# Kernel optimization log

Measured on AMD Instinct MI355X. Metric: run time of the kernel, lower is better.

Reference implementation:

```python
import jax, jax.numpy as jnp
import numpy as np

V, E, H, B, TE, TD = 32000, 256, 256, 32, 128, 64


def _gru_cell(x, h, Wi, Wh, bi, bh):
    # PyTorch GRU gate order: r, z, n
    gi = x @ Wi.T + bi            # [B, 3H]
    gh = h @ Wh.T + bh            # [B, 3H]
    i_r, i_z, i_n = jnp.split(gi, 3, axis=-1)
    h_r, h_z, h_n = jnp.split(gh, 3, axis=-1)
    r = jax.nn.sigmoid(i_r + h_r)
    z = jax.nn.sigmoid(i_z + h_z)
    n = jnp.tanh(i_n + r * h_n)
    return (1.0 - z) * n + z * h


def _run_gru(x_seq, h0, Wi, Wh, bi, bh, reverse=False):
    # x_seq: [B, T, D] -> outputs [B, T, H]
    xs = jnp.swapaxes(x_seq, 0, 1)  # [T, B, D]
    def step(h, x_t):
        h = _gru_cell(x_t, h, Wi, Wh, bi, bh)
        return h, h
    _, ys = jax.lax.scan(step, h0, xs, reverse=reverse)
    return jnp.swapaxes(ys, 0, 1)


def setup_inputs() -> dict:
    key = jax.random.key(0)
    ks = jax.random.split(key, 22)
    k = 1.0 / np.sqrt(H)
    u = lambda kk, shape, a: jax.random.uniform(kk, shape, jnp.float32, -a, a)
    return {
        'enc_in': jax.random.randint(ks[0], (B, TE), 0, V),
        'dec_in': jax.random.randint(ks[1], (B, TD), 0, V),
        'embed_W': u(ks[2], (V, E), 0.1),
        'Wi_f': u(ks[3], (3 * H, E), k), 'Wh_f': u(ks[4], (3 * H, H), k),
        'bi_f': u(ks[5], (3 * H,), k), 'bh_f': u(ks[6], (3 * H,), k),
        'Wi_b': u(ks[7], (3 * H, E), k), 'Wh_b': u(ks[8], (3 * H, H), k),
        'bi_b': u(ks[9], (3 * H,), k), 'bh_b': u(ks[10], (3 * H,), k),
        'Wi_d': u(ks[11], (3 * H, E + 2 * H), k), 'Wh_d': u(ks[12], (3 * H, H), k),
        'bi_d': u(ks[13], (3 * H,), k), 'bh_d': u(ks[14], (3 * H,), k),
        'W1_w': u(ks[15], (H, 2 * H), 1.0 / np.sqrt(2 * H)), 'W1_b': u(ks[16], (H,), 1.0 / np.sqrt(2 * H)),
        'W2_w': u(ks[17], (2 * H, H), k), 'W2_b': u(ks[18], (2 * H,), k),
        'lin_w': u(ks[19], (V, H), 0.1), 'lin_b': jnp.zeros((V,), jnp.float32),
    }


def reference(enc_in, dec_in, embed_W, Wi_f, Wh_f, bi_f, bh_f, Wi_b, Wh_b, bi_b, bh_b,
              Wi_d, Wh_d, bi_d, bh_d, W1_w, W1_b, W2_w, W2_b, lin_w, lin_b):
    # ---- encoder (bidirectional GRU, 1 layer) ----
    enc_emb = embed_W[enc_in]                                   # [B, TE, E]
    h0 = jnp.zeros((B, H), enc_emb.dtype)
    out_f = _run_gru(enc_emb, h0, Wi_f, Wh_f, bi_f, bh_f)       # [B, TE, H]
    out_b = _run_gru(enc_emb, h0, Wi_b, Wh_b, bi_b, bh_b, reverse=True)
    encoded = jnp.concatenate([out_f, out_b], axis=-1)          # [B, TE, 2H]

    # last valid state per example: encoded[i, sizes[i]-1]
    sizes = (enc_in > 0).sum(axis=1)                            # [B]
    last_states = encoded[jnp.arange(B), sizes - 1]             # [B, 2H]

    # ---- decoder with Luong attention (teacher forcing) ----
    dec_emb = embed_W[dec_in]                                   # [B, TD, E]
    h_init = last_states @ W1_w.T + W1_b                        # [B, H]
    ctx_init = jnp.zeros((B, 2 * H), enc_emb.dtype)

    def dec_step(carry, x_t):
        h, ctx = carry
        inp = jnp.concatenate([ctx, x_t], axis=-1)              # [B, E+2H]
        h = _gru_cell(inp, h, Wi_d, Wh_d, bi_d, bh_d)           # [B, H]
        comp = h @ W2_w.T + W2_b                                # [B, 2H]
        scores = jax.nn.softmax(jnp.einsum('bte,be->bt', encoded, comp), axis=-1)
        ctx = jnp.einsum('bt,bte->be', scores, encoded)          # [B, 2H]
        return (h, ctx), h

    _, outs = jax.lax.scan(dec_step, (h_init, ctx_init), jnp.swapaxes(dec_emb, 0, 1))
    outs = jnp.swapaxes(outs, 0, 1)                             # [B, TD, H]
    logits = outs @ lin_w.T + lin_b                             # [B, TD, V]
    return logits
```

## Files before the change

### kernel.cpp

```cpp
#include <hip/hip_runtime.h>
#include <hip/hip_bf16.h>

#define Vv 32000
#define Ee 256
#define Hh 256
#define Bb 32
#define TEe 128
#define TDd 64

typedef __attribute__((ext_vector_type(4))) float f32x4;
typedef __attribute__((ext_vector_type(8))) short short8;
typedef __attribute__((ext_vector_type(2))) unsigned int uint2v;
typedef __attribute__((ext_vector_type(4))) unsigned int uint4v;

static __device__ __forceinline__ unsigned short f2bf(float f){
  unsigned u = __float_as_uint(f);
  u += 0x7fffu + ((u >> 16) & 1u);
  return (unsigned short)(u >> 16);
}
static __device__ __forceinline__ unsigned pack2(float a, float b){
  return ((unsigned)f2bf(b) << 16) | (unsigned)f2bf(a);
}
static __device__ __forceinline__ float dot8(uint4v u, const float* hh){
  float s = 0.f;
  #pragma unroll
  for (int i = 0; i < 4; ++i){
    unsigned w = u[i];
    s = fmaf(__uint_as_float(w << 16),        hh[2*i],   s);
    s = fmaf(__uint_as_float(w & 0xffff0000u), hh[2*i+1], s);
  }
  return s;
}
static __device__ __forceinline__ float sigmoidf_(float x){
  return 1.f / (1.f + __expf(-x));
}
static __device__ __forceinline__ void gload16(const void* g, void* l){
  __builtin_amdgcn_global_load_lds((const __attribute__((address_space(1))) void*)g,
                                   (__attribute__((address_space(3))) void*)l, 16, 0, 0);
}

__global__ void k_prep(const float* __restrict__ Wh_f, const float* __restrict__ Wh_b,
                       const float* __restrict__ Wh_d,
                       const float* __restrict__ Wi_f, const float* __restrict__ Wi_b,
                       const float* __restrict__ Wi_d, const float* __restrict__ W2_w,
                       unsigned short* __restrict__ whf, unsigned short* __restrict__ whb,
                       unsigned short* __restrict__ whd,
                       unsigned short* __restrict__ wif, unsigned short* __restrict__ wib,
                       unsigned short* __restrict__ wid, unsigned short* __restrict__ w2t){
  int idx = blockIdx.x * 256 + threadIdx.x;
  if (idx < 589824){
    int which = idx / 196608, local = idx % 196608;
    int i = local & 7, r = (local >> 3) % 768, kb = local / 6144;
    const float* src = (which == 0) ? Wh_f : (which == 1) ? Wh_b : Wh_d;
    unsigned short* dst = (which == 0) ? whf : (which == 1) ? whb : whd;
    dst[local] = f2bf(src[(size_t)r*256 + kb*8 + i]);
  } else if (idx < 786432)   wif[idx - 589824] = f2bf(Wi_f[idx - 589824]);
  else if (idx < 983040)     wib[idx - 786432] = f2bf(Wi_b[idx - 786432]);
  else if (idx < 1572864)    wid[idx - 983040] = f2bf(Wi_d[idx - 983040]);
  else if (idx < 1703936){
    int l = idx - 1572864;
    int n = l >> 9, k = l & 511;
    w2t[l] = f2bf(W2_w[k*256 + n]);
  }
}

template<bool A_BF16, bool A_GATHER, bool B_BF16, int OUTMODE>
__global__ __launch_bounds__(256) void k_gemm(
  const void* __restrict__ Av, const int* __restrict__ tokp, const float* __restrict__ embp,
  const void* __restrict__ Bv,
  const float* __restrict__ bias, void* __restrict__ Cv,
  int M, int N, int K, int lda, int ldb, int ldc)
{
  __shared__ unsigned short lA[128*40];
  __shared__ unsigned short lB[128*40];
  const int SA = A_BF16 ? 32 : 40;
  const int SB = B_BF16 ? 32 : 40;
  const int tid  = threadIdx.x;
  const int lane = tid & 63;
  const int wv   = tid >> 6;
  const int w = tid >> 6, wr = w >> 1, wc = w & 1;
  const int m0 = blockIdx.y * 128, n0 = blockIdx.x * 128;
  f32x4 acc[4][4];
  #pragma unroll
  for (int i = 0; i < 4; ++i)
    #pragma unroll
    for (int j = 0; j < 4; ++j) acc[i][j] = (f32x4){0.f,0.f,0.f,0.f};

  for (int k0 = 0; k0 < K; k0 += 32){
    if (A_GATHER){
      #pragma unroll
      for (int it = 0; it < 4; ++it){
        int idx = tid + it*256; int r = idx >> 3, q = idx & 7;
        const float* src = embp + (size_t)tokp[m0 + r]*256 + k0 + q*4;
        f32x4 v = *(const f32x4*)src;
        uint2v pk; pk[0] = pack2(v[0], v[1]); pk[1] = pack2(v[2], v[3]);
        *(uint2v*)&lA[r*40 + q*4] = pk;
      }
    } else if (A_BF16){
      const unsigned short* A = (const unsigned short*)Av;
      #pragma unroll
      for (int i = 0; i < 2; ++i){
        const int rowb = (wv*2 + i)*16;
        gload16(A + (size_t)(m0 + rowb + (lane >> 2))*lda + k0 + (lane & 3)*8,
                &lA[rowb*32]);
      }
    } else {
      const float* A = (const float*)Av;
      #pragma unroll
      for (int it = 0; it < 4; ++it){
        int idx = tid + it*256; int r = idx >> 3, q = idx & 7;
        f32x4 v = *(const f32x4*)(A + (size_t)(m0+r)*lda + k0 + q*4);
        uint2v pk; pk[0] = pack2(v[0], v[1]); pk[1] = pack2(v[2], v[3]);
        *(uint2v*)&lA[r*40 + q*4] = pk;
      }
    }
    if (B_BF16){
      const unsigned short* Bp = (const unsigned short*)Bv;
      #pragma unroll
      for (int i = 0; i < 2; ++i){
        const int rowb = (wv*2 + i)*16;
        gload16(Bp + (size_t)(n0 + rowb + (lane >> 2))*ldb + k0 + (lane & 3)*8,
                &lB[rowb*32]);
      }
    } else {
      const float* Bp = (const float*)Bv;
      #pragma unroll
      for (int it = 0; it < 4; ++it){
        int idx = tid + it*256; int r = idx >> 3, q = idx & 7;
        f32x4 v = *(const f32x4*)(Bp + (size_t)(n0+r)*ldb + k0 + q*4);
        uint2v pk; pk[0] = pack2(v[0], v[1]); pk[1] = pack2(v[2], v[3]);
        *(uint2v*)&lB[r*40 + q*4] = pk;
      }
    }
    __syncthreads();
    short8 av[4], bv[4];
    #pragma unroll
    for (int i = 0; i < 4; ++i)
      av[i] = *(const short8*)&lA[(wr*64 + i*16 + (lane&15))*SA + (lane>>4)*8];
    #pragma unroll
    for (int j = 0; j < 4; ++j)
      bv[j] = *(const short8*)&lB[(wc*64 + j*16 + (lane&15))*SB + (lane>>4)*8];
    #pragma unroll
    for (int i = 0; i < 4; ++i)
      #pragma unroll
      for (int j = 0; j < 4; ++j)
        acc[i][j] = __builtin_amdgcn_mfma_f32_16x16x32_bf16(av[i], bv[j], acc[i][j], 0, 0, 0);
    __syncthreads();
  }
  #pragma unroll
  for (int i = 0; i < 4; ++i){
    #pragma unroll
    for (int j = 0; j < 4; ++j){
      int col = n0 + wc*64 + j*16 + (lane & 15);
      float bb = bias ? bias[col] : 0.f;
      #pragma unroll
      for (int r = 0; r < 4; ++r){
        int row = m0 + wr*64 + i*16 + (lane>>4)*4 + r;
        float v = acc[i][j][r] + bb;
        if (OUTMODE == 2){
          ((unsigned short*)Cv)[(size_t)(row >> 7)*98304 + (size_t)((row & 127) >> 3)*6144
                                + (size_t)col*8 + (row & 7)] = f2bf(v);
        } else if (OUTMODE == 1){
          ((unsigned short*)Cv)[(size_t)row*ldc + col] = f2bf(v);
        } else {
          ((float*)Cv)[(size_t)row*ldc + col] = v;
        }
      }
    }
  }
}

__global__ __launch_bounds__(1024) void k_encoder(
  const unsigned short* __restrict__ Whf, const unsigned short* __restrict__ Whb,
  const float* __restrict__ bhf, const float* __restrict__ bhb,
  const float* __restrict__ gif, const float* __restrict__ gib,
  float* __restrict__ encoded, unsigned short* __restrict__ encoded_bf,
  const float* __restrict__ lin_w, unsigned short* __restrict__ lin_bf, int do_lin)
{
  if (blockIdx.x >= 64){
    if (do_lin){
      const int nlin = Vv*Hh;
      for (int i = (blockIdx.x - 64)*1024 + threadIdx.x; i < nlin; i += 128*1024)
        lin_bf[i] = f2bf(lin_w[i]);
    }
    return;
  }
  extern __shared__ char smem[];
  unsigned short* lw = (unsigned short*)smem;
  float* hA   = (float*)(smem + 131072);
  float* hB   = (float*)(smem + 132096);
  float* parA = (float*)(smem + 133120);
  float* parB = (float*)(smem + 137216);
  const int dir = blockIdx.x & 1, b = blockIdx.x >> 1;
  const unsigned short* Wh = dir ? Whb : Whf;
  const float* bh = dir ? bhb : bhf;
  const float* gi = dir ? gib : gif;
  const int T = threadIdx.x;
  const int rl = T & 255, q4 = T >> 8;
  const int rrh = T & 511, hf = T >> 9;
  const unsigned short* wsrc = Wh + (size_t)(hf*16)*6144 + (size_t)(256 + rrh)*8;
  uint4v wb[8];
  #pragma unroll
  for (int d = 0; d < 8; ++d) wb[d] = *(const uint4v*)(wsrc + (size_t)d*6144);
  for (int cc = T; cc < 256*32; cc += 1024){
    int r = cc >> 5, q = cc & 31;
    *(uint4v*)&lw[(r*32 + (q ^ (r & 31)))*8] = *(const uint4v*)(Wh + (size_t)q*6144 + r*8);
  }
  float bh0 = 0.f, bh1 = 0.f, bh2 = 0.f;
  if (T < 256){ bh0 = bh[T]; bh1 = bh[T+256]; bh2 = bh[T+512]; hA[T] = 0.f; }
  __syncthreads();
  const float* hc = hA; float* hn = hB;
  for (int s = 0; s < TEe; ++s){
    const int t = dir ? (TEe-1-s) : s;
    float g0 = 0.f, g1 = 0.f, g2 = 0.f;
    if (T < 256){
      const float* grow = gi + (size_t)(b*TEe + t)*768;
      g0 = grow[T]; g1 = grow[T+256]; g2 = grow[T+512];
    }
    float aL = 0.f;
    #pragma unroll
    for (int i = 0; i < 8; ++i){
      const int ck = q4*8 + i;
      float hr[8];
      *(f32x4*)&hr[0] = *(const f32x4*)&hc[ck*8];
      *(f32x4*)&hr[4] = *(const f32x4*)&hc[ck*8+4];
      aL += dot8(*(const uint4v*)&lw[(rl*32 + (ck ^ (rl & 31)))*8], hr);
    }
    parA[q4*256 + rl] = aL;
    float aR = 0.f;
    const float* hh = hc + hf*128;
    #pragma unroll
    for (int q = 0; q < 16; ++q){
      float hr[8];
      *(f32x4*)&hr[0] = *(const f32x4*)&hh[q*8];
      *(f32x4*)&hr[4] = *(const f32x4*)&hh[q*8+4];
      aR += dot8(wb[q & 7], hr);
      wb[q & 7] = *(const uint4v*)(wsrc + (size_t)((q < 8) ? (q + 8) : (q - 8))*6144);
    }
    parB[hf*512 + rrh] = aR;
    __syncthreads();
    if (T < 256){
      const int j = T;
      const float A0 = parA[j] + parA[256+j] + parA[512+j] + parA[768+j] + bh0;
      const float A1 = parB[j] + parB[512+j] + bh1;
      const float A2 = parB[256+j] + parB[768+j] + bh2;
      const float r = sigmoidf_(g0 + A0);
      const float z = sigmoidf_(g1 + A1);
      const float n = tanhf(g2 + r*A2);
      const float hnew = (1.f - z)*n + z*hc[j];
      hn[j] = hnew;
      const size_t off = (size_t)(b*TEe + t)*512 + dir*256 + j;
      encoded[off] = hnew;
      encoded_bf[off] = f2bf(hnew);
    }
    __syncthreads();
    const float* tmp = hc; hc = hn; hn = (float*)tmp;
  }
}

__global__ __launch_bounds__(256) void k_post(
  const float* __restrict__ encoded, const float* __restrict__ W2b, float* __restrict__ encb2,
  const int* __restrict__ enc_in, const float* __restrict__ W1w, const float* __restrict__ W1b,
  float* __restrict__ h0)
{
  if (blockIdx.x < 1024){
    const int r = blockIdx.x*4 + (threadIdx.x >> 6), l = threadIdx.x & 63;
    const float* e = encoded + (size_t)r*512;
    float s = 0.f;
    for (int k = l; k < 512; k += 64) s += e[k]*W2b[k];
    for (int off = 32; off; off >>= 1) s += __shfl_down(s, off);
    if (l == 0) encb2[r] = s;
  } else {
    const int b = blockIdx.x - 1024, o = threadIdx.x;
    int c = 0;
    for (int t = 0; t < TEe; ++t) c += (enc_in[b*TEe + t] > 0);
    int idx = c - 1;
    idx = idx < 0 ? 0 : (idx > TEe-1 ? TEe-1 : idx);
    const float* ls = encoded + (size_t)(b*TEe + idx)*512;
    const float* wv = W1w + (size_t)o*512;
    float s = W1b[o];
    for (int k = 0; k < 512; k += 4){
      f32x4 a = *(const f32x4*)(ls + k);
      f32x4 w4 = *(const f32x4*)(wv + k);
      s = fmaf(a[0],w4[0], fmaf(a[1],w4[1], fmaf(a[2],w4[2], fmaf(a[3],w4[3], s))));
    }
    h0[b*256 + o] = s;
  }
}

#define DLR 128
__global__ __launch_bounds__(512, 1) void k_decoder(
  const unsigned short* __restrict__ Whd, const float* __restrict__ bhd,
  const float* __restrict__ gidx,
  const unsigned short* __restrict__ encw2,
  const float* __restrict__ encb2,
  const unsigned short* __restrict__ projt,
  const float* __restrict__ h0,
  unsigned short* __restrict__ outs_bf)
{
  extern __shared__ char smem[];
  unsigned short* le = (unsigned short*)smem;
  unsigned short* lw = (unsigned short*)(smem + 65536);
  float* h    = (float*)(smem + 131072);
  float* parL = (float*)(smem + 132096);
  float* parS1= (float*)(smem + 134144);
  float* parS2= (float*)(smem + 136192);
  float* gcs  = (float*)(smem + 138240);
  float* cpar = (float*)(smem + 140288);
  float* p    = (float*)(smem + 142336);
  float* ebl  = (float*)(smem + 142848);
  const int b = blockIdx.x, T = threadIdx.x;
  const unsigned short* ptc = projt + (size_t)b*98304;
  const unsigned short* wsrcM = Whd + (size_t)(DLR + T)*8;
  const int trow = 640 + (T >> 2), tq = (T & 3)*8;
  const unsigned short* wsrcT = Whd + (size_t)trow*8;
  const unsigned short* csrcM = ptc + (size_t)T*8;
  const int crow = 512 + (T >> 1), cq = (T & 1)*8;
  const unsigned short* csrcT = ptc + (size_t)crow*8;
  uint4v wb[8], wb2[2], cb[4], cb2[2];
  #pragma unroll
  for (int d = 0; d < 8; ++d) wb[d] = *(const uint4v*)(wsrcM + (size_t)d*6144);
  wb2[0] = *(const uint4v*)(wsrcT + (size_t)tq*6144);
  wb2[1] = *(const uint4v*)(wsrcT + (size_t)(tq+1)*6144);
  #pragma unroll
  for (int d = 0; d < 4; ++d) cb[d] = *(const uint4v*)(csrcM + (size_t)d*6144);
  cb2[0] = *(const uint4v*)(csrcT + (size_t)cq*6144);
  cb2[1] = *(const uint4v*)(csrcT + (size_t)(cq+1)*6144);
  for (int cc = T; cc < 128*32; cc += 512){
    int r = cc >> 5, q = cc & 31;
    *(uint4v*)&le[(r*32 + (q ^ (r & 31)))*8] =
        *(const uint4v*)(encw2 + ((size_t)(b*TEe + r) << 8) + (q << 3));
  }
  for (int cc = T; cc < DLR*32; cc += 512){
    int r = cc >> 5, q = cc & 31;
    *(uint4v*)&lw[(r*32 + (q ^ (r & 31)))*8] =
        *(const uint4v*)(Whd + (size_t)q*6144 + r*8);
  }
  for (int i = T; i < 256; i += 512) h[i] = h0[b*256 + i];
  gcs[T] = 0.f; cpar[T] = 0.f;
  if (T < TEe) ebl[T] = encb2[b*TEe + T];
  float bh0 = 0.f, bh1 = 0.f, bh2 = 0.f;
  if (T < 256){ bh0 = bhd[T]; bh1 = bhd[T+256]; bh2 = bhd[T+512]; }
  __syncthreads();
  float g0 = 0.f, g1 = 0.f, g2 = 0.f;
  if (T < 256){
    const float* grow = gidx + (size_t)(b*TDd)*768;
    g0 = grow[T]; g1 = grow[T+256]; g2 = grow[T+512];
  }
  #define DOTS_BODY                                                            \
  {                                                                            \
    { const int rL2 = T >> 2, qb2 = (T & 3)*8;                                 \
      const unsigned short* lwr = lw + rL2*256;                                \
      float a = 0.f;                                                           \
      _Pragma("unroll")                                                        \
      for (int i = 0; i < 8; ++i){                                             \
        const int q = qb2 + i;                                                 \
        float hr[8];                                                           \
        *(f32x4*)&hr[0] = *(const f32x4*)&h[q*8];                              \
        *(f32x4*)&hr[4] = *(const f32x4*)&h[q*8+4];                            \
        a += dot8(*(const uint4v*)(lwr + ((q ^ (rL2 & 31)) << 3)), hr);        \
      }                                                                        \
      parL[(T & 3)*128 + rL2] = a;                                             \
    }                                                                          \
    { float a = 0.f;                                                           \
      _Pragma("unroll")                                                        \
      for (int q = 0; q < 32; ++q){                                            \
        float hr[8];                                                           \
        *(f32x4*)&hr[0] = *(const f32x4*)&h[q*8];                              \
        *(f32x4*)&hr[4] = *(const f32x4*)&h[q*8+4];                            \
        a += dot8(wb[q & 7], hr);                                              \
        wb[q & 7] = *(const uint4v*)(wsrcM + (size_t)((q < 24) ? (q + 8) : (q - 24))*6144); \
      }                                                                        \
      parS1[T] = a;                                                            \
    }                                                                          \
    { float a = 0.f;                                                           \
      _Pragma("unroll")                                                        \
      for (int i = 0; i < 8; ++i){                                             \
        const int q = tq + i;                                                  \
        float hr[8];                                                           \
        *(f32x4*)&hr[0] = *(const f32x4*)&h[q*8];                              \
        *(f32x4*)&hr[4] = *(const f32x4*)&h[q*8+4];                            \
        a += dot8(wb2[i & 1], hr);                                             \
        wb2[i & 1] = *(const uint4v*)(wsrcT + (size_t)(tq + ((i < 6) ? (i + 2) : (i - 6)))*6144); \
      }                                                                        \
      parS2[(T & 3)*128 + (T >> 2)] = a;                                       \
    }                                                                          \
  }
  DOTS_BODY
  __syncthreads();
  for (int t = 0; t < TDd; ++t){
    if (T < 256){
      const int j = T;
      float A0, A2;
      if (j < 128){
        A0 = parL[j] + parL[128+j] + parL[256+j] + parL[384+j];
        A2 = parS1[384+j];
      } else {
        A0 = parS1[j-128];
        A2 = parS2[j-128] + parS2[j] + parS2[j+128] + parS2[j+256];
      }
      const float A1 = parS1[128+j];
      const float gcr = gcs[j];
      const float gcz = gcs[256+j];
      const float gcn = cpar[j] + cpar[256+j];
      const float r = sigmoidf_(g0 + gcr + A0 + bh0);
      const float z = sigmoidf_(g1 + gcz + A1 + bh1);
      const float n = tanhf(g2 + gcn + r*(A2 + bh2));
      const float hnew = (1.f - z)*n + z*h[j];
      h[j] = hnew;
      outs_bf[(size_t)(b*TDd + t)*256 + j] = f2bf(hnew);
    }
    if (t + 1 == TDd) break;
    __syncthreads();
    if (T < 256){
      const float* grow = gidx + (size_t)(b*TDd + t + 1)*768;
      g0 = grow[T]; g1 = grow[T+256]; g2 = grow[T+512];
    }
    DOTS_BODY
    {
      const int pos = T >> 2, kq = (T & 3)*8;
      const unsigned short* er = le + pos*256;
      float s = 0.f;
      #pragma unroll
      for (int i = 0; i < 8; ++i){
        const int q = kq + i;
        float hr[8];
        *(f32x4*)&hr[0] = *(const f32x4*)&h[q*8];
        *(f32x4*)&hr[4] = *(const f32x4*)&h[q*8+4];
        s += dot8(*(const uint4v*)(er + ((q ^ (pos & 31)) << 3)), hr);
      }
      s += __shfl_xor(s, 1);
      s += __shfl_xor(s, 2);
      if ((T & 3) == 0) p[pos] = s + ebl[pos];
    }
    __syncthreads();
    if (T < 64){
      float m = fmaxf(p[T], p[T+64]);
      for (int off = 32; off; off >>= 1) m = fmaxf(m, __shfl_xor(m, off));
      float e0 = __expf(p[T] - m), e1 = __expf(p[T+64] - m);
      float ss = e0 + e1;
      for (int off = 32; off; off >>= 1) ss += __shfl_xor(ss, off);
      float inv = 1.f / ss;
      p[T] = e0*inv; p[T+64] = e1*inv;
    }
    __syncthreads();
    {
      float c = 0.f;
      #pragma unroll
      for (int q = 0; q < 16; ++q){
        float pr[8];
        *(f32x4*)&pr[0] = *(const f32x4*)&p[q*8];
        *(f32x4*)&pr[4] = *(const f32x4*)&p[q*8+4];
        c += dot8(cb[q & 3], pr);
        cb[q & 3] = *(const uint4v*)(csrcM + (size_t)((q < 12) ? (q + 4) : (q - 12))*6144);
      }
      gcs[T] = c;
      float c2 = 0.f;
      #pragma unroll
      for (int i = 0; i < 8; ++i){
        const int q = cq + i;
        float pr[8];
        *(f32x4*)&pr[0] = *(const f32x4*)&p[q*8];
        *(f32x4*)&pr[4] = *(const f32x4*)&p[q*8+4];
        c2 += dot8(cb2[i & 1], pr);
        cb2[i & 1] = *(const uint4v*)(csrcT + (size_t)(cq + ((i < 6) ? (i + 2) : (i - 6)))*6144);
      }
      cpar[(T & 1)*256 + (T >> 1)] = c2;
    }
    __syncthreads();
  }
  #undef DOTS_BODY
}

extern "C" void kernel_launch(void* const* d_in, const int* in_sizes, int n_in,
                              void* d_out, int out_size, void* d_ws, size_t ws_size,
                              hipStream_t stream)
{
  (void)in_sizes; (void)n_in; (void)out_size;
  const int*   enc_in = (const int*)d_in[0];
  const int*   dec_in = (const int*)d_in[1];
  const float* embW   = (const float*)d_in[2];
  const float* Wi_f   = (const float*)d_in[3];
  const float* Wh_f   = (const float*)d_in[4];
  const float* bi_f   = (const float*)d_in[5];
  const float* bh_f   = (const float*)d_in[6];
  const float* Wi_b   = (const float*)d_in[7];
  const float* Wh_b   = (const float*)d_in[8];
  const float* bi_b   = (const float*)d_in[9];
  const float* bh_b   = (const float*)d_in[10];
  const float* Wi_d   = (const float*)d_in[11];
  const float* Wh_d   = (const float*)d_in[12];
  const float* bi_d   = (const float*)d_in[13];
  const float* bh_d   = (const float*)d_in[14];
  const float* W1_w   = (const float*)d_in[15];
  const float* W1_b   = (const float*)d_in[16];
  const float* W2_w   = (const float*)d_in[17];
  const float* W2_b   = (const float*)d_in[18];
  const float* lin_w  = (const float*)d_in[19];
  const float* lin_b  = (const float*)d_in[20];

  char* scr = (char*)d_out;
  float* gi_f    = (float*)(scr + 3145728);
  float* gi_b    = (float*)(scr + 15728640);
  float* gi_dx   = (float*)(scr + 28311552);
  float* enc     = (float*)(scr + 34603008);
  unsigned short* enc_bf  = (unsigned short*)(scr + 42991616);
  unsigned short* whf_bf = (unsigned short*)(scr + 53477376);
  unsigned short* whb_bf = (unsigned short*)(scr + 53870592);
  unsigned short* whd_bf = (unsigned short*)(scr + 54263808);
  unsigned short* encw2  = (unsigned short*)(scr + 54657024);
  unsigned short* projt  = (unsigned short*)(scr + 56754176);
  unsigned short* wif_bf = (unsigned short*)(scr + 63045632);
  unsigned short* wib_bf = (unsigned short*)(scr + 63438848);
  unsigned short* wid_bf = (unsigned short*)(scr + 63832064);
  unsigned short* w2t_bf = (unsigned short*)(scr + 65011712);
  float* encb2 = (float*)(scr + 65273856);
  float* h0    = (float*)(scr + 65290368);

  unsigned short* outs_bf = (unsigned short*)d_ws;
  unsigned short* lin_bf  = (unsigned short*)((char*)d_ws + (1<<20));
  const bool big = ws_size >= (size_t)(1<<20) + 16384000u + 1024u;

  hipFuncSetAttribute((const void*)k_encoder, hipFuncAttributeMaxDynamicSharedMemorySize, 141312);
  hipFuncSetAttribute((const void*)k_decoder, hipFuncAttributeMaxDynamicSharedMemorySize, 143360);

  k_prep<<<6656, 256, 0, stream>>>(Wh_f, Wh_b, Wh_d, Wi_f, Wi_b, Wi_d, W2_w,
                                   whf_bf, whb_bf, whd_bf, wif_bf, wib_bf, wid_bf, w2t_bf);

  k_gemm<false,true,true,0><<<dim3(6,32), 256, 0, stream>>>(
      nullptr, enc_in, embW, wif_bf, bi_f, gi_f, 4096, 768, 256, 0, 256, 768);
  k_gemm<false,true,true,0><<<dim3(6,32), 256, 0, stream>>>(
      nullptr, enc_in, embW, wib_bf, bi_b, gi_b, 4096, 768, 256, 0, 256, 768);
  k_gemm<false,true,true,0><<<dim3(6,16), 256, 0, stream>>>(
      nullptr, dec_in, embW, wid_bf + 512, bi_d, gi_dx, 2048, 768, 256, 0, 768, 768);

  k_encoder<<<192, 1024, 141312, stream>>>(whf_bf, whb_bf, bh_f, bh_b, gi_f, gi_b,
                                           enc, enc_bf, lin_w, lin_bf, big ? 1 : 0);
  k_post<<<1056, 256, 0, stream>>>(enc, W2_b, encb2, enc_in, W1_w, W1_b, h0);

  k_gemm<true,false,true,1><<<dim3(2,32), 256, 0, stream>>>(
      enc_bf, nullptr, nullptr, w2t_bf, nullptr, encw2, 4096, 256, 512, 512, 512, 256);
  k_gemm<true,false,true,2><<<dim3(6,32), 256, 0, stream>>>(
      enc_bf, nullptr, nullptr, wid_bf, nullptr, projt, 4096, 768, 512, 512, 768, 0);

  k_decoder<<<Bb, 512, 143360, stream>>>(whd_bf, bh_d, gi_dx, encw2, encb2, projt, h0, outs_bf);

  if (big)
    k_gemm<true,false,true,0><<<dim3(250,16), 256, 0, stream>>>(
        outs_bf, nullptr, nullptr, lin_bf, lin_b, d_out, 2048, 32000, 256, 256, 256, 32000);
  else
    k_gemm<true,false,false,0><<<dim3(250,16), 256, 0, stream>>>(
        outs_bf, nullptr, nullptr, lin_w, lin_b, d_out, 2048, 32000, 256, 256, 256, 32000);
}
```

Measured before the change: 1.629 ms.

## Fold decoder input-projection GEMM into idle encoder kernel blocks

The separate launch that computes the decoder's embedding input projection (gi_dx) is removed. That GEMM now runs inside k_encoder on 96 extra blocks (64..159), in parallel with the sequential GRU recurrence blocks, and the lin_w bf16 conversion moves to blocks 160+. The aim is to drop a kernel launch and hide the GEMM under the latency-bound encoder recurrence. The cost is that these GEMM blocks use 1024-thread blocks with only 256 threads active and the large dynamic shared allocation, which wastes resources and may reduce throughput of the conversion blocks.

```diff
diff --git a/kernel.cpp b/kernel.cpp
--- a/kernel.cpp
+++ b/kernel.cpp
@@ -77,8 +77,8 @@
   const int SB = B_BF16 ? 32 : 40;
   const int tid  = threadIdx.x;
   const int lane = tid & 63;
-  const int wv   = tid >> 6;
-  const int w = tid >> 6, wr = w >> 1, wc = w & 1;
+  const int wvv  = tid >> 6;
+  const int wr = wvv >> 1, wc = wvv & 1;
   const int m0 = blockIdx.y * 128, n0 = blockIdx.x * 128;
   f32x4 acc[4][4];
   #pragma unroll
@@ -100,7 +100,7 @@
       const unsigned short* A = (const unsigned short*)Av;
       #pragma unroll
       for (int i = 0; i < 2; ++i){
-        const int rowb = (wv*2 + i)*16;
+        const int rowb = (wvv*2 + i)*16;
         gload16(A + (size_t)(m0 + rowb + (lane >> 2))*lda + k0 + (lane & 3)*8,
                 &lA[rowb*32]);
       }
@@ -118,7 +118,7 @@
       const unsigned short* Bp = (const unsigned short*)Bv;
       #pragma unroll
       for (int i = 0; i < 2; ++i){
-        const int rowb = (wv*2 + i)*16;
+        const int rowb = (wvv*2 + i)*16;
         gload16(Bp + (size_t)(n0 + rowb + (lane >> 2))*ldb + k0 + (lane & 3)*8,
                 &lB[rowb*32]);
       }
@@ -175,17 +175,85 @@
   const float* __restrict__ bhf, const float* __restrict__ bhb,
   const float* __restrict__ gif, const float* __restrict__ gib,
   float* __restrict__ encoded, unsigned short* __restrict__ encoded_bf,
-  const float* __restrict__ lin_w, unsigned short* __restrict__ lin_bf, int do_lin)
+  const float* __restrict__ lin_w, unsigned short* __restrict__ lin_bf, int do_lin,
+  const int* __restrict__ dec_in, const float* __restrict__ embW,
+  const unsigned short* __restrict__ wid_bf, const float* __restrict__ bi_d,
+  float* __restrict__ gi_dx)
 {
-  if (blockIdx.x >= 64){
+  extern __shared__ char smem[];
+  if (blockIdx.x >= 160){
     if (do_lin){
       const int nlin = Vv*Hh;
-      for (int i = (blockIdx.x - 64)*1024 + threadIdx.x; i < nlin; i += 128*1024)
+      for (int i = (blockIdx.x - 160)*1024 + threadIdx.x; i < nlin; i += 32*1024)
         lin_bf[i] = f2bf(lin_w[i]);
     }
     return;
   }
-  extern __shared__ char smem[];
+  if (blockIdx.x >= 64){
+    unsigned short* lA = (unsigned short*)smem;
+    unsigned short* lB = (unsigned short*)(smem + 16384);
+    const int g = blockIdx.x - 64;
+    const int m0 = (g & 15)*128, n0 = (g >> 4)*128;
+    const int tid = threadIdx.x;
+    const int lane = tid & 63, wvv = tid >> 6;
+    const int wr = wvv >> 1, wc = wvv & 1;
+    const unsigned short* Bp = wid_bf + 512;
+    f32x4 acc[4][4];
+    #pragma unroll
+    for (int i = 0; i < 4; ++i)
+      #pragma unroll
+      for (int j = 0; j < 4; ++j) acc[i][j] = (f32x4){0.f,0.f,0.f,0.f};
+    for (int k0 = 0; k0 < 256; k0 += 32){
+      if (tid < 256){
+        #pragma unroll
+        for (int it = 0; it < 4; ++it){
+          int idx = tid + it*256; int r = idx >> 3, q = idx & 7;
+          const float* src = embW + (size_t)dec_in[m0 + r]*256 + k0 + q*4;
+          f32x4 v = *(const f32x4*)src;
+          uint2v pk; pk[0] = pack2(v[0], v[1]); pk[1] = pack2(v[2], v[3]);
+          *(uint2v*)&lA[r*40 + q*4] = pk;
+        }
+        #pragma unroll
+        for (int i = 0; i < 2; ++i){
+          const int rowb = (wvv*2 + i)*16;
+          gload16(Bp + (size_t)(n0 + rowb + (lane >> 2))*768 + k0 + (lane & 3)*8,
+                  &lB[rowb*32]);
+        }
+      }
+      __syncthreads();
+      if (tid < 256){
+        short8 av[4], bv[4];
+        #pragma unroll
+        for (int i = 0; i < 4; ++i)
+          av[i] = *(const short8*)&lA[(wr*64 + i*16 + (lane&15))*40 + (lane>>4)*8];
+        #pragma unroll
+        for (int j = 0; j < 4; ++j)
+          bv[j] = *(const short8*)&lB[(wc*64 + j*16 + (lane&15))*32 + (lane>>4)*8];
+        #pragma unroll
+        for (int i = 0; i < 4; ++i)
+          #pragma unroll
+          for (int j = 0; j < 4; ++j)
+            acc[i][j] = __builtin_amdgcn_mfma_f32_16x16x32_bf16(av[i], bv[j], acc[i][j], 0, 0, 0);
+      }
+      __syncthreads();
+    }
+    if (tid < 256){
+      #pragma unroll
+      for (int i = 0; i < 4; ++i){
+        #pragma unroll
+        for (int j = 0; j < 4; ++j){
+          int col = n0 + wc*64 + j*16 + (lane & 15);
+          float bb = bi_d[col];
+          #pragma unroll
+          for (int r = 0; r < 4; ++r){
+            int row = m0 + wr*64 + i*16 + (lane>>4)*4 + r;
+            gi_dx[(size_t)row*768 + col] = acc[i][j][r] + bb;
+          }
+        }
+      }
+    }
+    return;
+  }
   unsigned short* lw = (unsigned short*)smem;
   float* hA   = (float*)(smem + 131072);
   float* hB   = (float*)(smem + 132096);
@@ -531,11 +599,10 @@
       nullptr, enc_in, embW, wif_bf, bi_f, gi_f, 4096, 768, 256, 0, 256, 768);
   k_gemm<false,true,true,0><<<dim3(6,32), 256, 0, stream>>>(
       nullptr, enc_in, embW, wib_bf, bi_b, gi_b, 4096, 768, 256, 0, 256, 768);
-  k_gemm<false,true,true,0><<<dim3(6,16), 256, 0, stream>>>(
-      nullptr, dec_in, embW, wid_bf + 512, bi_d, gi_dx, 2048, 768, 256, 0, 768, 768);
 
   k_encoder<<<192, 1024, 141312, stream>>>(whf_bf, whb_bf, bh_f, bh_b, gi_f, gi_b,
-                                           enc, enc_bf, lin_w, lin_bf, big ? 1 : 0);
+                                           enc, enc_bf, lin_w, lin_bf, big ? 1 : 0,
+                                           dec_in, embW, wid_bf, bi_d, gi_dx);
   k_post<<<1056, 256, 0, stream>>>(enc, W2_b, encb2, enc_in, W1_w, W1_b, h0);
 
   k_gemm<true,false,true,1><<<dim3(2,32), 256, 0, stream>>>(
```

Result: no change. 1.648 ms (+1.2%).
